# Optimization experiments

Hardware: AMD Instinct MI355X
Metric: run time of the kernel (lower is better)

## Reference

```python
import jax, jax.numpy as jnp
import numpy as np

B, L, S, H, D = 4, 2048, 2048, 8, 64


def setup_inputs() -> dict:
    key = jax.random.key(0)
    kq, kk, kv = jax.random.split(key, 3)
    queries = jax.random.normal(kq, (B, L, H, D), dtype=jnp.float32)
    keys = jax.random.normal(kk, (B, S, H, D), dtype=jnp.float32)
    values = jax.random.normal(kv, (B, S, H, D), dtype=jnp.float32)
    # causal mask: True = masked (positions j > i), broadcast to [B, L, S]
    causal = jnp.triu(jnp.ones((L, S), dtype=bool), k=1)
    attn_mask = jnp.broadcast_to(causal, (B, L, S))
    return {"queries": queries, "keys": keys, "values": values, "attn_mask": attn_mask}


def reference(queries, keys, values, attn_mask):
    # queries: [B,L,H,D], keys/values: [B,S,H,D], attn_mask: [B,L,S] bool (True=masked)
    D_ = queries.shape[-1]
    scale = 1.0 / jnp.sqrt(jnp.asarray(D_, dtype=queries.dtype))
    scores = jnp.einsum('blhd,bshd->bhls', queries, keys) * scale  # [B,H,L,S]
    scores = jnp.where(attn_mask[:, None, :, :], -jnp.inf, scores)
    attn = jax.nn.softmax(scores, axis=-1)  # dropout p=0.0 (eval) -> identity
    context = jnp.einsum('bhls,bshd->blhd', attn, values)  # [B,L,H,D]
    return (context, attn)
```

## Files before the change

### kernel.cpp

```cpp
#include <hip/hip_runtime.h>
#include <cstdint>
#include <cstddef>

#define BB 4
#define LL 2048
#define SS 2048
#define HH 8
#define DD 64
#define TQ 64
#define TK 64
#define HD (HH*DD)
#define CTX_N (BB*LL*HH*DD)
#define NBH (BB*HH)
#define NJT (SS/TK)
#define WS_NEED ((size_t)2 * NBH * SS * DD * 2)

using f32x4  = __attribute__((ext_vector_type(4))) float;
using bf16x8 = __attribute__((ext_vector_type(8))) short;
using s16x4  = __attribute__((ext_vector_type(4))) short;

__device__ __forceinline__ short f2bf(float f) {
  union { float f; unsigned u; } v; v.f = f;
  unsigned r = v.u + 0x7FFFu + ((v.u >> 16) & 1u);
  return (short)(r >> 16);
}

__device__ __forceinline__ void bar_lds() {
  asm volatile("s_waitcnt lgkmcnt(0)" ::: "memory");
  __builtin_amdgcn_s_barrier();
}

__launch_bounds__(256, 4)
__global__ void prep(const float* __restrict__ K, const float* __restrict__ V,
                     short* __restrict__ Kbs, short* __restrict__ Vts) {
  __shared__ float Vl[64][68];
  const int tid = threadIdx.x, bid = blockIdx.x;
  const int bh = bid >> 5, jt = bid & 31;
  const int b = bh >> 3, h = bh & 7;
  const int j0 = jt * 64;
  const int row = tid >> 2, q = tid & 3;

  {
    const float* kp = K + ((size_t)(b*SS + j0 + row)*HH + h)*DD + q*16;
    short* kout = Kbs + ((size_t)bh*SS + j0 + row)*DD + q*16;
    #pragma unroll
    for (int c2 = 0; c2 < 2; ++c2) {
      bf16x8 o;
      #pragma unroll
      for (int i = 0; i < 8; ++i) o[i] = f2bf(kp[c2*8 + i]);
      *(bf16x8*)(kout + c2*8) = o;
    }
  }
  {
    const float* vp = V + ((size_t)(b*SS + j0 + row)*HH + h)*DD + q*16;
    #pragma unroll
    for (int i = 0; i < 4; ++i)
      *(float4*)&Vl[row][q*16 + 4*i] = *(const float4*)(vp + 4*i);
  }
  __syncthreads();
  {
    const int d = tid >> 2, jq = tid & 3;
    short* vout = Vts + (((size_t)bh*NJT + jt)*DD + d)*TK;
    #pragma unroll
    for (int c2 = 0; c2 < 2; ++c2) {
      const int c = jq*2 + c2;
      bf16x8 o;
      #pragma unroll
      for (int i = 0; i < 8; ++i) o[i] = f2bf(Vl[c*8 + i][d]);
      *(bf16x8*)(vout + c*8) = o;
    }
  }
}

__launch_bounds__(256, 4)
__global__ void fa_fwd(const float* __restrict__ Qg,
                       const short* __restrict__ Kbs,
                       const short* __restrict__ Vts,
                       float* __restrict__ Out) {
  __shared__ short Kl[TK*DD];
  __shared__ short Vtl[DD*TK];
  __shared__ float pf[4][16][68];

  const int tid  = threadIdx.x;
  const int wv   = tid >> 6;
  const int lane = tid & 63;
  const int g    = lane >> 4;
  const int r16  = lane & 15;

  const int bid = blockIdx.x;
  const int u   = bid >> 5;
  const int bh  = bid & 31;
  const int u1  = u >> 3, u0 = u & 7;
  const int qrank = (u1 == 0) ? u0 : (u1 == 1) ? (31 - u0) : (u1 == 2) ? (15 - u0) : (16 + u0);
  const int b = bh >> 3, h = bh & 7;
  const int q0  = (31 - qrank) * TQ;
  const int nkt = 32 - qrank;

  const size_t attn_base = (size_t)CTX_N + (size_t)bh * (size_t)LL * (size_t)SS;

  {
    const int jz = q0 + TQ;
    const int n4 = (SS - jz) >> 2;
    if (n4 > 0) {
      f32x4 z = {0.f, 0.f, 0.f, 0.f};
      for (int row = 0; row < TQ; ++row) {
        float* rp = Out + attn_base + (size_t)(q0 + row) * SS + jz;
        for (int c = tid; c < n4; c += 256)
          __builtin_nontemporal_store(z, (f32x4*)(rp + 4*c));
      }
    }
  }

  const float qscale = 0.125f * 1.44269504088896f;
  const float* qptr  = Qg + (size_t)(b*LL + q0 + wv*16 + r16)*HD + h*DD;
  bf16x8 aQ[2];
  #pragma unroll
  for (int s = 0; s < 2; ++s)
    #pragma unroll
    for (int i = 0; i < 8; ++i)
      aQ[s][i] = f2bf(qptr[s*32 + g*8 + i] * qscale);

  auto stage_k = [&](int kt) {
    const short* Kt = Kbs + ((size_t)bh*SS + kt*TK)*DD;
    #pragma unroll
    for (int i = 0; i < 2; ++i) {
      const int ci = wv*128 + i*64 + lane;
      const int row = ci >> 3, c = ci & 7;
      const bf16x8 kv = *(const bf16x8*)(Kt + ci*8);
      *(bf16x8*)((char*)Kl + row*128 + ((c ^ (row & 7)) << 4)) = kv;
    }
  };
  auto stage_v = [&](int kt) {
    const short* Vt = Vts + ((size_t)bh*NJT + kt)*DD*TK;
    #pragma unroll
    for (int i = 0; i < 2; ++i) {
      const int ci = wv*128 + i*64 + lane;
      const int row = ci >> 3, c = ci & 7;
      const bf16x8 vv = *(const bf16x8*)(Vt + ci*8);
      *(bf16x8*)((char*)Vtl + row*128 + ((c ^ (row & 7)) << 4)) = vv;
    }
  };

  auto qk = [&](int j0t, f32x4 (&sacc)[4], bool diag) {
    const int sw = r16 & 7;
    #pragma unroll
    for (int jt = 0; jt < 4; ++jt) {
      const char* base = (const char*)Kl + (jt*16 + r16)*128;
      const bf16x8 bk0 = *(const bf16x8*)(base + (((g    ) ^ sw) << 4));
      const bf16x8 bk1 = *(const bf16x8*)(base + (((4 + g) ^ sw) << 4));
      f32x4 a = {0.f, 0.f, 0.f, 0.f};
      a = __builtin_amdgcn_mfma_f32_16x16x32_bf16(aQ[0], bk0, a, 0, 0, 0);
      a = __builtin_amdgcn_mfma_f32_16x16x32_bf16(aQ[1], bk1, a, 0, 0, 0);
      if (diag) {
        const int jabs = j0t + jt*16 + r16;
        #pragma unroll
        for (int r = 0; r < 4; ++r)
          if (jabs > q0 + wv*16 + g*4 + r) a[r] = -1e30f;
      }
      sacc[jt] = a;
    }
  };

  float lpart[4] = {0.f, 0.f, 0.f, 0.f};
  for (int kt = 0; kt < nkt; ++kt) {
    bar_lds();
    stage_k(kt);
    bar_lds();
    f32x4 sacc[4];
    qk(kt * TK, sacc, kt == nkt - 1);
    #pragma unroll
    for (int jt = 0; jt < 4; ++jt)
      #pragma unroll
      for (int r = 0; r < 4; ++r)
        lpart[r] += __builtin_exp2f(sacc[jt][r]);
  }
  float invl[4];
  #pragma unroll
  for (int r = 0; r < 4; ++r) {
    #pragma unroll
    for (int msk = 1; msk < 16; msk <<= 1)
      lpart[r] += __shfl_xor(lpart[r], msk, 64);
    invl[r] = 1.0f / lpart[r];
  }

  f32x4 ctx[4];
  #pragma unroll
  for (int dt = 0; dt < 4; ++dt) ctx[dt] = (f32x4){0.f, 0.f, 0.f, 0.f};

  for (int kt = 0; kt < nkt; ++kt) {
    const int j0 = kt * TK;
    bar_lds();
    stage_k(kt);
    stage_v(kt);
    bar_lds();

    f32x4 sacc[4];
    qk(j0, sacc, kt == nkt - 1);

    #pragma unroll
    for (int jt = 0; jt < 4; ++jt)
      #pragma unroll
      for (int r = 0; r < 4; ++r)
        pf[wv][g*4 + r][jt*16 + r16] = __builtin_exp2f(sacc[jt][r]) * invl[r];

    #pragma unroll
    for (int rg = 0; rg < 4; ++rg) {
      const int row = rg*4 + g;
      const f32x4 p4 = *(const f32x4*)&pf[wv][row][r16*4];
      __builtin_nontemporal_store(p4,
        (f32x4*)(Out + attn_base + (size_t)(q0 + wv*16 + row)*SS + j0 + r16*4));
    }

    const int sw = r16 & 7;
    #pragma unroll
    for (int ks = 0; ks < 2; ++ks) {
      const f32x4 pa0 = *(const f32x4*)&pf[wv][r16][ks*32 + g*8];
      const f32x4 pa1 = *(const f32x4*)&pf[wv][r16][ks*32 + g*8 + 4];
      bf16x8 pa;
      #pragma unroll
      for (int i = 0; i < 4; ++i) { pa[i] = f2bf(pa0[i]); pa[4+i] = f2bf(pa1[i]); }
      #pragma unroll
      for (int dt = 0; dt < 4; ++dt) {
        const char* vbase = (const char*)Vtl + (dt*16 + r16)*128;
        const bf16x8 vb = *(const bf16x8*)(vbase + (((ks*4 + g) ^ sw) << 4));
        ctx[dt] = __builtin_amdgcn_mfma_f32_16x16x32_bf16(pa, vb, ctx[dt], 0, 0, 0);
      }
    }
  }

  #pragma unroll
  for (int dt = 0; dt < 4; ++dt)
    #pragma unroll
    for (int r = 0; r < 4; ++r)
      pf[wv][g*4 + r][dt*16 + r16] = ctx[dt][r];
  #pragma unroll
  for (int rg = 0; rg < 4; ++rg) {
    const int row = rg*4 + g;
    const f32x4 c4 = *(const f32x4*)&pf[wv][row][r16*4];
    __builtin_nontemporal_store(c4,
      (f32x4*)(Out + (size_t)(b*LL + q0 + wv*16 + row)*HD + h*DD + r16*4));
  }
}

struct SU {
  union {
    float vs[TK][68];
    float pf[4][16][68];
  };
};

__launch_bounds__(256, 4)
__global__ void fa_fwd_lds(const float* __restrict__ Qg,
                           const float* __restrict__ Kg,
                           const float* __restrict__ Vg,
                           float* __restrict__ Out) {
  __shared__ short Kl[TK][72];
  __shared__ short Vt[DD][72];
  __shared__ SU U;

  const int tid  = threadIdx.x;
  const int wv   = tid >> 6;
  const int lane = tid & 63;
  const int g    = lane >> 4;
  const int r16  = lane & 15;

  const int bid   = blockIdx.x;
  const int qrank = bid >> 5;
  const int bh    = bid & 31;
  const int b     = bh >> 3;
  const int h     = bh & 7;
  const int q0    = (31 - qrank) * TQ;
  const int nkt   = (q0 / TK) + 1;

  const float* Kbh = Kg + (size_t)b*SS*HD + h*DD;
  const float* Vbh = Vg + (size_t)b*SS*HD + h*DD;
  const size_t attn_base = (size_t)CTX_N + (size_t)(b*HH + h) * (size_t)LL * (size_t)SS;

  {
    const int jz = q0 + TQ;
    const int n4 = (SS - jz) >> 2;
    if (n4 > 0) {
      f32x4 z = {0.f, 0.f, 0.f, 0.f};
      for (int row = 0; row < TQ; ++row) {
        float* rp = Out + attn_base + (size_t)(q0 + row) * SS + jz;
        for (int c = tid; c < n4; c += 256)
          __builtin_nontemporal_store(z, (f32x4*)(rp + 4*c));
      }
    }
  }

  const float qscale = 0.125f * 1.44269504088896f;
  const float* qptr  = Qg + (size_t)(b*LL + q0 + wv*16 + r16)*HD + h*DD;
  bf16x8 aQ[2];
  #pragma unroll
  for (int s = 0; s < 2; ++s)
    #pragma unroll
    for (int i = 0; i < 8; ++i)
      aQ[s][i] = f2bf(qptr[s*32 + g*8 + i] * qscale);

  auto stage_k = [&](int j0) {
    #pragma unroll
    for (int c = 0; c < 4; ++c) {
      const int chunk = tid + c*256;
      const int row = chunk >> 4, c4 = chunk & 15;
      const float4 kv = *(const float4*)(Kbh + (size_t)(j0 + row)*HD + c4*4);
      s16x4 s4; s4[0] = f2bf(kv.x); s4[1] = f2bf(kv.y); s4[2] = f2bf(kv.z); s4[3] = f2bf(kv.w);
      *(s16x4*)&Kl[row][c4*4] = s4;
    }
  };

  auto compute_s = [&](int j0, f32x4 (&sacc)[4], bool diag) {
    #pragma unroll
    for (int jt = 0; jt < 4; ++jt) {
      bf16x8 bk0 = *(const bf16x8*)&Kl[jt*16 + r16][g*8];
      bf16x8 bk1 = *(const bf16x8*)&Kl[jt*16 + r16][32 + g*8];
      f32x4 a = {0.f, 0.f, 0.f, 0.f};
      a = __builtin_amdgcn_mfma_f32_16x16x32_bf16(aQ[0], bk0, a, 0, 0, 0);
      a = __builtin_amdgcn_mfma_f32_16x16x32_bf16(aQ[1], bk1, a, 0, 0, 0);
      if (diag) {
        const int jabs = j0 + jt*16 + r16;
        #pragma unroll
        for (int r = 0; r < 4; ++r) {
          if (jabs > q0 + wv*16 + g*4 + r) a[r] = -1e30f;
        }
      }
      sacc[jt] = a;
    }
  };

  float lpart[4] = {0.f, 0.f, 0.f, 0.f};
  for (int kt = 0; kt < nkt; ++kt) {
    __syncthreads();
    stage_k(kt * TK);
    __syncthreads();
    f32x4 sacc[4];
    compute_s(kt * TK, sacc, kt == nkt - 1);
    #pragma unroll
    for (int r = 0; r < 4; ++r)
      #pragma unroll
      for (int jt = 0; jt < 4; ++jt)
        lpart[r] += __builtin_exp2f(sacc[jt][r]);
  }
  float invl[4];
  #pragma unroll
  for (int r = 0; r < 4; ++r) {
    #pragma unroll
    for (int msk = 1; msk < 16; msk <<= 1)
      lpart[r] += __shfl_xor(lpart[r], msk, 64);
    invl[r] = 1.0f / lpart[r];
  }

  f32x4 ctx[4];
  #pragma unroll
  for (int dt = 0; dt < 4; ++dt) ctx[dt] = (f32x4){0.f, 0.f, 0.f, 0.f};

  for (int kt = 0; kt < nkt; ++kt) {
    const int j0 = kt * TK;
    __syncthreads();
    stage_k(j0);
    #pragma unroll
    for (int c = 0; c < 4; ++c) {
      const int chunk = tid + c*256;
      const int row = chunk >> 4, c4 = chunk & 15;
      const float4 vv = *(const float4*)(Vbh + (size_t)(j0 + row)*HD + c4*4);
      *(float4*)&U.vs[row][c4*4] = vv;
    }
    __syncthreads();
    #pragma unroll
    for (int c = 0; c < 4; ++c) {
      const float4 vv = *(const float4*)&U.vs[lane][wv*16 + c*4];
      Vt[wv*16 + c*4 + 0][lane] = f2bf(vv.x);
      Vt[wv*16 + c*4 + 1][lane] = f2bf(vv.y);
      Vt[wv*16 + c*4 + 2][lane] = f2bf(vv.z);
      Vt[wv*16 + c*4 + 3][lane] = f2bf(vv.w);
    }
    __syncthreads();

    f32x4 sacc[4];
    compute_s(j0, sacc, kt == nkt - 1);

    #pragma unroll
    for (int jt = 0; jt < 4; ++jt)
      #pragma unroll
      for (int r = 0; r < 4; ++r)
        U.pf[wv][g*4 + r][jt*16 + r16] = __builtin_exp2f(sacc[jt][r]) * invl[r];

    #pragma unroll
    for (int rg = 0; rg < 4; ++rg) {
      const int row = rg*4 + g;
      const f32x4 p4 = *(const f32x4*)&U.pf[wv][row][r16*4];
      __builtin_nontemporal_store(p4,
        (f32x4*)(Out + attn_base + (size_t)(q0 + wv*16 + row)*SS + j0 + r16*4));
    }

    #pragma unroll
    for (int ks = 0; ks < 2; ++ks) {
      const f32x4 pa0 = *(const f32x4*)&U.pf[wv][r16][ks*32 + g*8];
      const f32x4 pa1 = *(const f32x4*)&U.pf[wv][r16][ks*32 + g*8 + 4];
      bf16x8 pa;
      #pragma unroll
      for (int i = 0; i < 4; ++i) { pa[i] = f2bf(pa0[i]); pa[4+i] = f2bf(pa1[i]); }
      #pragma unroll
      for (int dt = 0; dt < 4; ++dt) {
        bf16x8 vb = *(const bf16x8*)&Vt[dt*16 + r16][ks*32 + g*8];
        ctx[dt] = __builtin_amdgcn_mfma_f32_16x16x32_bf16(pa, vb, ctx[dt], 0, 0, 0);
      }
    }
  }

  #pragma unroll
  for (int dt = 0; dt < 4; ++dt)
    #pragma unroll
    for (int r = 0; r < 4; ++r)
      U.pf[wv][g*4 + r][dt*16 + r16] = ctx[dt][r];
  #pragma unroll
  for (int rg = 0; rg < 4; ++rg) {
    const int row = rg*4 + g;
    const f32x4 c4 = *(const f32x4*)&U.pf[wv][row][r16*4];
    __builtin_nontemporal_store(c4,
      (f32x4*)(Out + (size_t)(b*LL + q0 + wv*16 + row)*HD + h*DD + r16*4));
  }
}

extern "C" void kernel_launch(void* const* d_in, const int* in_sizes, int n_in,
                              void* d_out, int out_size, void* d_ws, size_t ws_size,
                              hipStream_t stream) {
  const float* Q = (const float*)d_in[0];
  const float* K = (const float*)d_in[1];
  const float* V = (const float*)d_in[2];
  float* Out = (float*)d_out;
  if (ws_size >= WS_NEED) {
    short* Kbs = (short*)d_ws;
    short* Vts = Kbs + (size_t)NBH*SS*DD;
    prep<<<dim3(NBH*NJT), dim3(256), 0, stream>>>(K, V, Kbs, Vts);
    fa_fwd<<<dim3(BB*HH*(LL/TQ)), dim3(256), 0, stream>>>(Q, Kbs, Vts, Out);
  } else {
    fa_fwd_lds<<<dim3(BB*HH*(LL/TQ)), dim3(256), 0, stream>>>(Q, K, V, Out);
  }
}
```

Measured before the change: 145.9 us.

## Double-buffer K tiles in LDS and load V fragments directly from global

Replaces the single K/V LDS tiles with a two-slot K buffer, prefetching the next K tile into registers while computing the current one and writing it to the other slot after compute. This removes one barrier per iteration in both passes. V is no longer staged through LDS; each wave reads its MFMA B-fragments straight from global memory. Each wave now fetches its own copy of the V tile, and the extra prefetch registers may reduce occupancy.

```diff
diff --git a/kernel.cpp b/kernel.cpp
--- a/kernel.cpp
+++ b/kernel.cpp
@@ -77,8 +77,7 @@
                        const short* __restrict__ Kbs,
                        const short* __restrict__ Vts,
                        float* __restrict__ Out) {
-  __shared__ short Kl[TK*DD];
-  __shared__ short Vtl[DD*TK];
+  __shared__ short Kb[2][TK*DD];
   __shared__ float pf[4][16][68];
 
   const int tid  = threadIdx.x;
@@ -120,32 +119,28 @@
     for (int i = 0; i < 8; ++i)
       aQ[s][i] = f2bf(qptr[s*32 + g*8 + i] * qscale);
 
-  auto stage_k = [&](int kt) {
-    const short* Kt = Kbs + ((size_t)bh*SS + kt*TK)*DD;
+  const short* Kbh = Kbs + (size_t)bh * SS * DD;
+
+  auto kload = [&](int t, bf16x8 (&kr)[2]) {
+    const short* Kt = Kbh + (size_t)t * TK * DD;
+    #pragma unroll
+    for (int i = 0; i < 2; ++i)
+      kr[i] = *(const bf16x8*)(Kt + (wv*128 + i*64 + lane)*8);
+  };
+  auto kwrite = [&](int bsel, const bf16x8 (&kr)[2]) {
     #pragma unroll
     for (int i = 0; i < 2; ++i) {
       const int ci = wv*128 + i*64 + lane;
       const int row = ci >> 3, c = ci & 7;
-      const bf16x8 kv = *(const bf16x8*)(Kt + ci*8);
-      *(bf16x8*)((char*)Kl + row*128 + ((c ^ (row & 7)) << 4)) = kv;
-    }
-  };
-  auto stage_v = [&](int kt) {
-    const short* Vt = Vts + ((size_t)bh*NJT + kt)*DD*TK;
-    #pragma unroll
-    for (int i = 0; i < 2; ++i) {
-      const int ci = wv*128 + i*64 + lane;
-      const int row = ci >> 3, c = ci & 7;
-      const bf16x8 vv = *(const bf16x8*)(Vt + ci*8);
-      *(bf16x8*)((char*)Vtl + row*128 + ((c ^ (row & 7)) << 4)) = vv;
-    }
-  };
-
-  auto qk = [&](int j0t, f32x4 (&sacc)[4], bool diag) {
+      *(bf16x8*)((char*)Kb[bsel] + row*128 + ((c ^ (row & 7)) << 4)) = kr[i];
+    }
+  };
+
+  auto qk = [&](const short* KL, int j0t, f32x4 (&sacc)[4], bool diag) {
     const int sw = r16 & 7;
     #pragma unroll
     for (int jt = 0; jt < 4; ++jt) {
-      const char* base = (const char*)Kl + (jt*16 + r16)*128;
+      const char* base = (const char*)KL + (jt*16 + r16)*128;
       const bf16x8 bk0 = *(const bf16x8*)(base + (((g    ) ^ sw) << 4));
       const bf16x8 bk1 = *(const bf16x8*)(base + (((4 + g) ^ sw) << 4));
       f32x4 a = {0.f, 0.f, 0.f, 0.f};
@@ -161,18 +156,25 @@
     }
   };
 
+  {
+    bf16x8 kr[2];
+    kload(0, kr);
+    kwrite(0, kr);
+  }
   float lpart[4] = {0.f, 0.f, 0.f, 0.f};
-  for (int kt = 0; kt < nkt; ++kt) {
+  for (int t = 0; t < nkt; ++t) {
     bar_lds();
-    stage_k(kt);
-    bar_lds();
+    const bool more = (t + 1 < nkt);
+    bf16x8 kr[2];
+    if (more) kload(t + 1, kr);
     f32x4 sacc[4];
-    qk(kt * TK, sacc, kt == nkt - 1);
+    qk(Kb[t & 1], t * TK, sacc, t == nkt - 1);
     #pragma unroll
     for (int jt = 0; jt < 4; ++jt)
       #pragma unroll
       for (int r = 0; r < 4; ++r)
         lpart[r] += __builtin_exp2f(sacc[jt][r]);
+    if (more) kwrite((t + 1) & 1, kr);
   }
   float invl[4];
   #pragma unroll
@@ -187,15 +189,29 @@
   #pragma unroll
   for (int dt = 0; dt < 4; ++dt) ctx[dt] = (f32x4){0.f, 0.f, 0.f, 0.f};
 
-  for (int kt = 0; kt < nkt; ++kt) {
-    const int j0 = kt * TK;
+  bar_lds();
+  {
+    bf16x8 kr[2];
+    kload(0, kr);
+    kwrite(0, kr);
+  }
+  for (int t = 0; t < nkt; ++t) {
+    const int j0 = t * TK;
     bar_lds();
-    stage_k(kt);
-    stage_v(kt);
-    bar_lds();
+    const bool more = (t + 1 < nkt);
+    bf16x8 kr[2];
+    if (more) kload(t + 1, kr);
+
+    const short* Vt = Vts + ((size_t)bh*NJT + t)*DD*TK;
+    bf16x8 vb[2][4];
+    #pragma unroll
+    for (int ks = 0; ks < 2; ++ks)
+      #pragma unroll
+      for (int dt = 0; dt < 4; ++dt)
+        vb[ks][dt] = *(const bf16x8*)(Vt + (dt*16 + r16)*TK + ks*32 + g*8);
 
     f32x4 sacc[4];
-    qk(j0, sacc, kt == nkt - 1);
+    qk(Kb[t & 1], j0, sacc, t == nkt - 1);
 
     #pragma unroll
     for (int jt = 0; jt < 4; ++jt)
@@ -211,7 +227,6 @@
         (f32x4*)(Out + attn_base + (size_t)(q0 + wv*16 + row)*SS + j0 + r16*4));
     }
 
-    const int sw = r16 & 7;
     #pragma unroll
     for (int ks = 0; ks < 2; ++ks) {
       const f32x4 pa0 = *(const f32x4*)&pf[wv][r16][ks*32 + g*8];
@@ -220,12 +235,11 @@
       #pragma unroll
       for (int i = 0; i < 4; ++i) { pa[i] = f2bf(pa0[i]); pa[4+i] = f2bf(pa1[i]); }
       #pragma unroll
-      for (int dt = 0; dt < 4; ++dt) {
-        const char* vbase = (const char*)Vtl + (dt*16 + r16)*128;
-        const bf16x8 vb = *(const bf16x8*)(vbase + (((ks*4 + g) ^ sw) << 4));
-        ctx[dt] = __builtin_amdgcn_mfma_f32_16x16x32_bf16(pa, vb, ctx[dt], 0, 0, 0);
-      }
-    }
+      for (int dt = 0; dt < 4; ++dt)
+        ctx[dt] = __builtin_amdgcn_mfma_f32_16x16x32_bf16(pa, vb[ks][dt], ctx[dt], 0, 0, 0);
+    }
+
+    if (more) kwrite((t + 1) & 1, kr);
   }
 
   #pragma unroll
```

Measured after the change: 152.9 us. 1.05x slower.
